# Kernel optimization log

Measured on AMD Instinct MI355X. Metric: run time of the kernel, lower is better.

## Reference

```python
import jax, jax.numpy as jnp
import numpy as np

N_HEAD = 4
HEAD_DIM = 32
D_MODEL = 128
NEG_BIG = -1.0e9  # note: source uses (mask-1)*(-1e9), reproduced faithfully
LN_EPS = 1e-05


def _layer_norm(x, gain, bias):
    mean = jnp.mean(x, axis=-1, keepdims=True)
    var = jnp.mean(jnp.square(x - mean), axis=-1, keepdims=True)
    return gain * (x - mean) / jnp.sqrt(var + LN_EPS) + bias


def setup_inputs() -> dict:
    key = jax.random.key(0)
    ks = jax.random.split(key, 6)
    L, S, D = 8, 2048, D_MODEL
    x = jax.random.normal(ks[0], (L, S, D), dtype=jnp.float32)
    mask = jnp.ones((L, S), dtype=jnp.int32)
    qkv_w = jax.random.normal(ks[1], (D, 3 * D), dtype=jnp.float32) * (1.0 / np.sqrt(D))
    out_w = jax.random.normal(ks[2], (D, D), dtype=jnp.float32) * (1.0 / np.sqrt(D))
    w1 = jax.random.normal(ks[3], (D, 384), dtype=jnp.float32) * (1.0 / np.sqrt(D))
    b1 = jnp.zeros((384,), dtype=jnp.float32)
    w2 = jax.random.normal(ks[4], (384, D), dtype=jnp.float32) * (1.0 / np.sqrt(384))
    b2 = jnp.zeros((D,), dtype=jnp.float32)
    g1 = jnp.ones((D,), dtype=jnp.float32)
    be1 = jnp.zeros((D,), dtype=jnp.float32)
    g2 = jnp.ones((D,), dtype=jnp.float32)
    be2 = jnp.zeros((D,), dtype=jnp.float32)
    return {"x": x, "mask": mask, "qkv_w": qkv_w, "out_w": out_w,
            "w1": w1, "b1": b1, "w2": w2, "b2": b2,
            "g1": g1, "be1": be1, "g2": g2, "be2": be2}


def reference(x, mask, qkv_w, out_w, w1, b1, w2, b2, g1, be1, g2, be2):
    # x: [L, S, D] -- the python list axis of the original module is L (each element batch=1)
    L, S, D = x.shape
    H, hd = N_HEAD, HEAD_DIM
    m = mask.astype(jnp.float32)  # [L, S]

    # QKV projection (single shared weight, split into q/k/v)
    qkv = jnp.einsum('lsd,de->lse', x, qkv_w)  # [L, S, 3D]
    q, k, v = jnp.split(qkv, 3, axis=-1)
    q = q.reshape(L, S, H, hd).transpose(0, 2, 1, 3)  # [L, H, S, hd]
    k = k.reshape(L, S, H, hd).transpose(0, 2, 1, 3)
    v = v.reshape(L, S, H, hd).transpose(0, 2, 1, 3)

    scale = 1.0 / np.sqrt(D // H)
    scores = jnp.einsum('lhqd,lhkd->lhqk', q, k) * scale  # [L, H, S, S]

    # outer-product padding mask, faithful to source: amask*scores + (amask-1)*(-1e9)
    amask = (m[:, None, :, None] * m[:, None, None, :])  # [L, 1, S, S]
    masked = amask * scores + (amask - 1.0) * NEG_BIG
    attn = jax.nn.softmax(masked, axis=-1)

    ctx = jnp.einsum('lhqk,lhkd->lhqd', attn, v)  # [L, H, S, hd]
    ctx = ctx.transpose(0, 2, 1, 3).reshape(L, S, D)
    attn_out = jnp.einsum('lsd,de->lse', ctx, out_w)  # output projection

    # residual + LN1 (dropout rate 0.0 -> identity)
    h = _layer_norm(attn_out + x, g1, be1)

    # FFN: Dense(384, relu) -> Dense(128, relu)
    ff = jax.nn.relu(jnp.einsum('lsd,df->lsf', h, w1) + b1)
    ff = jax.nn.relu(jnp.einsum('lsf,fd->lsd', ff, w2) + b2)

    # residual + LN2
    out = _layer_norm(ff + h, g2, be2)
    return out
```

## Files before the change

kernel.cpp:

```cpp
#include <hip/hip_runtime.h>
#include <hip/hip_bf16.h>

typedef __attribute__((ext_vector_type(8))) short bf16x8;
typedef __attribute__((ext_vector_type(4))) float f32x4;
typedef unsigned short u16;
typedef unsigned int u32;

__device__ __forceinline__ u32 bfr(float x) {
  u32 u = __float_as_uint(x);
  return (u + 0x7fffu + ((u >> 16) & 1u)) >> 16;
}
__device__ __forceinline__ u32 pk2(float lo, float hi) {
  return bfr(lo) | (bfr(hi) << 16);
}
__device__ __forceinline__ u32 cvtpk(float lo, float hi) {
  u32 r;
  asm("v_cvt_pk_bf16_f32 %0, %1, %2" : "=v"(r) : "v"(lo), "v"(hi));
  return r;
}

__device__ __forceinline__ f32x4 mfma16(bf16x8 a, bf16x8 b, f32x4 c) {
  return __builtin_amdgcn_mfma_f32_16x16x32_bf16(a, b, c, 0, 0, 0);
}

__global__ __launch_bounds__(256) void prep_weights(
    const float* __restrict__ qkv_w, const float* __restrict__ out_w,
    const float* __restrict__ w1, const float* __restrict__ w2,
    u16* __restrict__ qkvT, u16* __restrict__ outT,
    u16* __restrict__ w1T, u16* __restrict__ w2T) {
  int idx = blockIdx.x * 256 + threadIdx.x;
  if (idx < 49152) {
    int n = idx >> 7, k = idx & 127;
    qkvT[idx] = (u16)bfr(qkv_w[k * 384 + n]);
  } else if (idx < 49152 + 16384) {
    int i = idx - 49152;
    int n = i >> 7, k = i & 127;
    outT[i] = (u16)bfr(out_w[k * 128 + n]);
  } else if (idx < 49152 + 16384 + 49152) {
    int i = idx - 49152 - 16384;
    int n = i >> 7, k = i & 127;
    w1T[i] = (u16)bfr(w1[k * 384 + n]);
  } else if (idx < 163840) {
    int i = idx - 49152 - 16384 - 49152;
    int n = i / 384, k = i - n * 384;
    w2T[i] = (u16)bfr(w2[k * 128 + n]);
  }
}

__global__ __launch_bounds__(256) void prep_x(const float* __restrict__ x,
                                              u16* __restrict__ xb) {
  int idx = blockIdx.x * 256 + threadIdx.x;
  const float4* p = (const float4*)(x + (size_t)idx * 8);
  float4 a = p[0], b = p[1];
  uint4 w = {pk2(a.x, a.y), pk2(a.z, a.w), pk2(b.x, b.y), pk2(b.z, b.w)};
  *(uint4*)(xb + (size_t)idx * 8) = w;
}

template <int K, int N, int EPI>
__global__ __launch_bounds__(256) void gemm_bf16(
    const u16* __restrict__ A, const u16* __restrict__ WT,
    const float* __restrict__ bias, float* __restrict__ C,
    u16* __restrict__ O0, u16* __restrict__ O1, u16* __restrict__ O2) {
  __shared__ u16 lds_a[64 * 136];
  __shared__ u16 lds_b[64 * 136];
  const int m0 = blockIdx.x * 64, n0 = blockIdx.y * 64;
  const int tid = threadIdx.x, lane = tid & 63, wv = tid >> 6;
  const int wm = wv >> 1, wn = wv & 1, c = lane & 15, g = lane >> 4;

  f32x4 acc[2][2] = {};
  for (int kt = 0; kt < K / 128; ++kt) {
    if (kt) __syncthreads();
    for (int i = tid; i < 1024; i += 256) {
      int row = i >> 4, cc = (i & 15) * 8;
      *(uint4*)(&lds_a[row * 136 + cc]) =
          *(const uint4*)(A + (size_t)(m0 + row) * K + kt * 128 + cc);
      *(uint4*)(&lds_b[row * 136 + cc]) =
          *(const uint4*)(WT + (size_t)(n0 + row) * K + kt * 128 + cc);
    }
    __syncthreads();
#pragma unroll
    for (int ks = 0; ks < 4; ++ks) {
      bf16x8 a0 = *(bf16x8*)(&lds_a[(wm * 32 + c) * 136 + ks * 32 + 8 * g]);
      bf16x8 a1 = *(bf16x8*)(&lds_a[(wm * 32 + 16 + c) * 136 + ks * 32 + 8 * g]);
      bf16x8 b0 = *(bf16x8*)(&lds_b[(wn * 32 + c) * 136 + ks * 32 + 8 * g]);
      bf16x8 b1 = *(bf16x8*)(&lds_b[(wn * 32 + 16 + c) * 136 + ks * 32 + 8 * g]);
      acc[0][0] = mfma16(a0, b0, acc[0][0]);
      acc[0][1] = mfma16(a0, b1, acc[0][1]);
      acc[1][0] = mfma16(a1, b0, acc[1][0]);
      acc[1][1] = mfma16(a1, b1, acc[1][1]);
    }
  }
#pragma unroll
  for (int mi = 0; mi < 2; ++mi)
#pragma unroll
    for (int ni = 0; ni < 2; ++ni) {
      const int n = n0 + wn * 32 + ni * 16 + c;
      const int mb = m0 + wm * 32 + mi * 16 + 4 * g;
      if constexpr (EPI == 0) {
#pragma unroll
        for (int r = 0; r < 4; ++r)
          C[(size_t)(mb + r) * N + n] = acc[mi][ni][r];
      } else if constexpr (EPI == 1) {
        float bv = bias[n];
#pragma unroll
        for (int r = 0; r < 4; ++r)
          C[(size_t)(mb + r) * N + n] = fmaxf(acc[mi][ni][r] + bv, 0.f);
      } else if constexpr (EPI == 2) {
        float bv = bias[n];
#pragma unroll
        for (int r = 0; r < 4; ++r)
          O0[(size_t)(mb + r) * N + n] =
              (u16)bfr(fmaxf(acc[mi][ni][r] + bv, 0.f));
      } else {
        const int reg = n >> 7, hh = (n >> 5) & 3, d = n & 31;
        const int l = mb >> 11, s = mb & 2047;
        const size_t lh = (size_t)l * 4 + hh;
        if (reg == 0) {
#pragma unroll
          for (int r = 0; r < 4; ++r)
            O0[(lh * 2048 + s + r) * 32 + d] =
                (u16)bfr(acc[mi][ni][r] * 0.17677669529663687f);
        } else if (reg == 1) {
#pragma unroll
          for (int r = 0; r < 4; ++r)
            O1[(lh * 2048 + s + r) * 32 + d] = (u16)bfr(acc[mi][ni][r]);
        } else {
          uint2 w = {pk2(acc[mi][ni][0], acc[mi][ni][1]),
                     pk2(acc[mi][ni][2], acc[mi][ni][3])};
          *(uint2*)(O2 + (lh * 32 + d) * 2048 + s) = w;
        }
      }
    }
}

__global__ __launch_bounds__(256) void attn2(
    const u16* __restrict__ Qs, const u16* __restrict__ Kb,
    const u16* __restrict__ Vt, const int* __restrict__ mask,
    u16* __restrict__ ctx) {
  __shared__ u16 lds_k[2][64 * 40];
  __shared__ u16 lds_vt[2][32 * 72];
  __shared__ u16 lds_p[4][16 * 72];
  __shared__ float lds_mk[2][64];

  const int bid = blockIdx.x;
  const int qt = bid & 31, lh = bid >> 5;
  const int tid = threadIdx.x, lane = tid & 63, wv = tid >> 6;
  const int c = lane & 15, g = lane >> 4;
  const int tok0 = (lh >> 2) * 2048;
  const int h = lh & 3;

  const int qrow = qt * 64 + wv * 16 + c;
  const bf16x8 qf = *(const bf16x8*)(Qs + ((size_t)lh * 2048 + qrow) * 32 + 8 * g);
  const float mq = (float)mask[tok0 + qrow];

  const int kr_ = tid & 63, kc_ = tid >> 6;
  const int vr_ = tid >> 3, vc_ = tid & 7;
  const u16* kbase = Kb + ((size_t)lh * 2048) * 32 + kr_ * 32 + kc_ * 8;
  const u16* vbase = Vt + ((size_t)lh * 32 + vr_) * 2048 + vc_ * 8;

  uint4 krg, vrg;
  float mkv;
  auto issue = [&](int kt0) {
    krg = *(const uint4*)(kbase + (size_t)kt0 * 32);
    vrg = *(const uint4*)(vbase + kt0);
    mkv = (tid < 64) ? (float)mask[tok0 + kt0 + tid] : 0.f;
  };
  auto commit = [&](int buf) {
    *(uint4*)(&lds_k[buf][kr_ * 40 + kc_ * 8]) = krg;
    *(uint4*)(&lds_vt[buf][vr_ * 72 + vc_ * 8]) = vrg;
    if (tid < 64) lds_mk[buf][tid] = mkv;
  };

  issue(0);
  commit(0);
  __syncthreads();

  f32x4 acc0 = {0.f, 0.f, 0.f, 0.f}, acc1 = {0.f, 0.f, 0.f, 0.f};
  float m_run = -1e30f, lsum = 0.f;
  const f32x4 zf = {0.f, 0.f, 0.f, 0.f};

  for (int t = 0; t < 32; ++t) {
    const int cur = t & 1;
    if (t < 31) issue((t + 1) * 64);

    f32x4 s[4];
#pragma unroll
    for (int j = 0; j < 4; ++j) {
      bf16x8 a = *(bf16x8*)(&lds_k[cur][(16 * j + c) * 40 + 8 * g]);
      s[j] = mfma16(a, qf, zf);
    }
    float sv[16];
#pragma unroll
    for (int j = 0; j < 4; ++j) {
      float4 mk4 = *(float4*)(&lds_mk[cur][16 * j + 4 * g]);
      const float* mkp = (const float*)&mk4;
#pragma unroll
      for (int r = 0; r < 4; ++r) {
        float am = mq * mkp[r];
        sv[4 * j + r] = am * s[j][r] + (am - 1.0f) * (-1e9f);
      }
    }
    float tmax = sv[0];
#pragma unroll
    for (int i = 1; i < 16; ++i) tmax = fmaxf(tmax, sv[i]);
    tmax = fmaxf(tmax, __shfl_xor(tmax, 16));
    tmax = fmaxf(tmax, __shfl_xor(tmax, 32));
    if (!__all(tmax <= m_run + 8.0f)) {
      float mnew = fmaxf(m_run, tmax);
      float corr = __expf(m_run - mnew);
      m_run = mnew;
      lsum *= corr;
      acc0 *= corr;
      acc1 *= corr;
    }
    float p[16], psum = 0.f;
#pragma unroll
    for (int i = 0; i < 16; ++i) {
      p[i] = __expf(sv[i] - m_run);
      psum += p[i];
    }
    lsum += psum;
#pragma unroll
    for (int j = 0; j < 4; ++j) {
      uint2 w = {cvtpk(p[4 * j], p[4 * j + 1]), cvtpk(p[4 * j + 2], p[4 * j + 3])};
      *(uint2*)(&lds_p[wv][c * 72 + 16 * j + 4 * g]) = w;
    }
    bf16x8 pb0 = *(bf16x8*)(&lds_p[wv][c * 72 + 8 * g]);
    bf16x8 pb1 = *(bf16x8*)(&lds_p[wv][c * 72 + 32 + 8 * g]);
    bf16x8 v00 = *(bf16x8*)(&lds_vt[cur][c * 72 + 8 * g]);
    bf16x8 v01 = *(bf16x8*)(&lds_vt[cur][c * 72 + 32 + 8 * g]);
    bf16x8 v10 = *(bf16x8*)(&lds_vt[cur][(16 + c) * 72 + 8 * g]);
    bf16x8 v11 = *(bf16x8*)(&lds_vt[cur][(16 + c) * 72 + 32 + 8 * g]);
    acc0 = mfma16(v00, pb0, acc0);
    acc0 = mfma16(v01, pb1, acc0);
    acc1 = mfma16(v10, pb0, acc1);
    acc1 = mfma16(v11, pb1, acc1);

    if (t < 31) commit(cur ^ 1);
    __syncthreads();
  }
  float lt = lsum;
  lt += __shfl_xor(lt, 16);
  lt += __shfl_xor(lt, 32);
  float inv = 1.0f / lt;
  u16* op = ctx + (size_t)(tok0 + qrow) * 128 + h * 32;
  uint2 o0 = {cvtpk(acc0[0] * inv, acc0[1] * inv),
              cvtpk(acc0[2] * inv, acc0[3] * inv)};
  uint2 o1 = {cvtpk(acc1[0] * inv, acc1[1] * inv),
              cvtpk(acc1[2] * inv, acc1[3] * inv)};
  *(uint2*)(op + 4 * g) = o0;
  *(uint2*)(op + 16 + 4 * g) = o1;
}

template <bool WB>
__global__ __launch_bounds__(256) void ln_res(
    const float* __restrict__ a, const float* __restrict__ b,
    const float* __restrict__ gain, const float* __restrict__ bias,
    float* __restrict__ out, u16* __restrict__ outb) {
  int token = blockIdx.x * 4 + (threadIdx.x >> 6);
  int lane = threadIdx.x & 63;
  const float2 av = *(const float2*)(a + (size_t)token * 128 + lane * 2);
  const float2 bv = *(const float2*)(b + (size_t)token * 128 + lane * 2);
  float x0 = av.x + bv.x, x1 = av.y + bv.y;
  float s = x0 + x1, q = x0 * x0 + x1 * x1;
#pragma unroll
  for (int off = 32; off >= 1; off >>= 1) {
    s += __shfl_xor(s, off);
    q += __shfl_xor(q, off);
  }
  float mean = s * (1.0f / 128.0f);
  float var = q * (1.0f / 128.0f) - mean * mean;
  float inv = rsqrtf(var + 1e-5f);
  float2 gv = *(const float2*)(gain + lane * 2);
  float2 bev = *(const float2*)(bias + lane * 2);
  float2 o = {gv.x * (x0 - mean) * inv + bev.x,
              gv.y * (x1 - mean) * inv + bev.y};
  *(float2*)(out + (size_t)token * 128 + lane * 2) = o;
  if constexpr (WB)
    *(u32*)(outb + (size_t)token * 128 + lane * 2) = pk2(o.x, o.y);
}

extern "C" void kernel_launch(void* const* d_in, const int* in_sizes, int n_in,
                              void* d_out, int out_size, void* d_ws,
                              size_t ws_size, hipStream_t stream) {
  (void)in_sizes; (void)n_in; (void)out_size; (void)ws_size;
  const float* x = (const float*)d_in[0];
  const int* mask = (const int*)d_in[1];
  const float* qkv_w = (const float*)d_in[2];
  const float* out_w = (const float*)d_in[3];
  const float* w1 = (const float*)d_in[4];
  const float* b1 = (const float*)d_in[5];
  const float* w2 = (const float*)d_in[6];
  const float* b2 = (const float*)d_in[7];
  const float* g1 = (const float*)d_in[8];
  const float* be1 = (const float*)d_in[9];
  const float* g2 = (const float*)d_in[10];
  const float* be2 = (const float*)d_in[11];
  float* out = (float*)d_out;

  char* ws = (char*)d_ws;
  const size_t MB = 1 << 20;
  u16* Qs = (u16*)(ws);
  u16* Kb = (u16*)(ws + 4 * MB);
  u16* Vt = (u16*)(ws + 8 * MB);
  u16* ff_bf = (u16*)(ws);
  u16* ctx_bf = (u16*)(ws + 12 * MB);
  float* attn_out = (float*)(ws + 16 * MB);
  float* ff2 = attn_out;
  float* h = (float*)(ws + 24 * MB);
  u16* h_bf = (u16*)(ws + 32 * MB);
  u16* x_bf = (u16*)(ws + 36 * MB);
  u16* qkvT = (u16*)(ws + 40 * MB);
  u16* outT = qkvT + 384 * 128;
  u16* w1T = outT + 128 * 128;
  u16* w2T = w1T + 384 * 128;

  prep_weights<<<640, 256, 0, stream>>>(qkv_w, out_w, w1, w2, qkvT, outT, w1T, w2T);
  prep_x<<<1024, 256, 0, stream>>>(x, x_bf);
  gemm_bf16<128, 384, 3><<<dim3(256, 6), 256, 0, stream>>>(
      x_bf, qkvT, nullptr, nullptr, Qs, Kb, Vt);
  attn2<<<1024, 256, 0, stream>>>(Qs, Kb, Vt, mask, ctx_bf);
  gemm_bf16<128, 128, 0><<<dim3(256, 2), 256, 0, stream>>>(
      ctx_bf, outT, nullptr, attn_out, nullptr, nullptr, nullptr);
  ln_res<true><<<4096, 256, 0, stream>>>(attn_out, x, g1, be1, h, h_bf);
  gemm_bf16<128, 384, 2><<<dim3(256, 6), 256, 0, stream>>>(
      h_bf, w1T, b1, nullptr, ff_bf, nullptr, nullptr);
  gemm_bf16<384, 128, 1><<<dim3(256, 2), 256, 0, stream>>>(
      ff_bf, w2T, b2, ff2, nullptr, nullptr, nullptr);
  ln_res<false><<<4096, 256, 0, stream>>>(ff2, h, g2, be2, out, nullptr);
}
```

Measured before the change: 114.3 us.

## Fuse residual-add and LayerNorm into full-row output and FFN2 GEMM epilogues

```diff
diff --git a/kernel.cpp b/kernel.cpp
--- a/kernel.cpp
+++ b/kernel.cpp
@@ -59,7 +59,7 @@
 template <int K, int N, int EPI>
 __global__ __launch_bounds__(256) void gemm_bf16(
     const u16* __restrict__ A, const u16* __restrict__ WT,
-    const float* __restrict__ bias, float* __restrict__ C,
+    const float* __restrict__ bias,
     u16* __restrict__ O0, u16* __restrict__ O1, u16* __restrict__ O2) {
   __shared__ u16 lds_a[64 * 136];
   __shared__ u16 lds_b[64 * 136];
@@ -96,16 +96,7 @@
     for (int ni = 0; ni < 2; ++ni) {
       const int n = n0 + wn * 32 + ni * 16 + c;
       const int mb = m0 + wm * 32 + mi * 16 + 4 * g;
-      if constexpr (EPI == 0) {
-#pragma unroll
-        for (int r = 0; r < 4; ++r)
-          C[(size_t)(mb + r) * N + n] = acc[mi][ni][r];
-      } else if constexpr (EPI == 1) {
-        float bv = bias[n];
-#pragma unroll
-        for (int r = 0; r < 4; ++r)
-          C[(size_t)(mb + r) * N + n] = fmaxf(acc[mi][ni][r] + bv, 0.f);
-      } else if constexpr (EPI == 2) {
+      if constexpr (EPI == 2) {
         float bv = bias[n];
 #pragma unroll
         for (int r = 0; r < 4; ++r)
@@ -131,6 +122,86 @@
         }
       }
     }
+}
+
+template <int K, bool RELU>
+__global__ __launch_bounds__(256) void gemm_ln(
+    const u16* __restrict__ A, const u16* __restrict__ WT,
+    const float* __restrict__ bias, const float* __restrict__ resid,
+    const float* __restrict__ gain, const float* __restrict__ lnb,
+    float* __restrict__ outf, u16* __restrict__ outb) {
+  __shared__ u16 lds_a[64 * 136];
+  __shared__ u16 lds_b[128 * 136];
+  const int m0 = blockIdx.x * 64;
+  const int tid = threadIdx.x, lane = tid & 63, wv = tid >> 6;
+  const int c = lane & 15, g = lane >> 4;
+
+  f32x4 acc[8] = {};
+  for (int kt = 0; kt < K / 128; ++kt) {
+    if (kt) __syncthreads();
+    for (int i = tid; i < 1024; i += 256) {
+      int row = i >> 4, cc = (i & 15) * 8;
+      *(uint4*)(&lds_a[row * 136 + cc]) =
+          *(const uint4*)(A + (size_t)(m0 + row) * K + kt * 128 + cc);
+    }
+    for (int i = tid; i < 2048; i += 256) {
+      int row = i >> 4, cc = (i & 15) * 8;
+      *(uint4*)(&lds_b[row * 136 + cc]) =
+          *(const uint4*)(WT + (size_t)row * K + kt * 128 + cc);
+    }
+    __syncthreads();
+#pragma unroll
+    for (int ks = 0; ks < 4; ++ks) {
+      bf16x8 a = *(bf16x8*)(&lds_a[(wv * 16 + c) * 136 + ks * 32 + 8 * g]);
+#pragma unroll
+      for (int ni = 0; ni < 8; ++ni) {
+        bf16x8 b = *(bf16x8*)(&lds_b[(ni * 16 + c) * 136 + ks * 32 + 8 * g]);
+        acc[ni] = mfma16(a, b, acc[ni]);
+      }
+    }
+  }
+  const int rbase = m0 + wv * 16 + 4 * g;
+  float gv[8], lb[8], bv[8];
+#pragma unroll
+  for (int ni = 0; ni < 8; ++ni) {
+    gv[ni] = gain[ni * 16 + c];
+    lb[ni] = lnb[ni * 16 + c];
+    if constexpr (RELU) bv[ni] = bias[ni * 16 + c];
+  }
+  float t[8][4];
+  float sum[4] = {0.f, 0.f, 0.f, 0.f}, sq[4] = {0.f, 0.f, 0.f, 0.f};
+#pragma unroll
+  for (int ni = 0; ni < 8; ++ni) {
+#pragma unroll
+    for (int r = 0; r < 4; ++r) {
+      float v = acc[ni][r];
+      if constexpr (RELU) v = fmaxf(v + bv[ni], 0.f);
+      v += resid[(size_t)(rbase + r) * 128 + ni * 16 + c];
+      t[ni][r] = v;
+      sum[r] += v;
+      sq[r] += v * v;
+    }
+  }
+#pragma unroll
+  for (int off = 1; off < 16; off <<= 1) {
+#pragma unroll
+    for (int r = 0; r < 4; ++r) {
+      sum[r] += __shfl_xor(sum[r], off);
+      sq[r] += __shfl_xor(sq[r], off);
+    }
+  }
+#pragma unroll
+  for (int r = 0; r < 4; ++r) {
+    float mean = sum[r] * (1.0f / 128.0f);
+    float var = sq[r] * (1.0f / 128.0f) - mean * mean;
+    float inv = rsqrtf(var + 1e-5f);
+#pragma unroll
+    for (int ni = 0; ni < 8; ++ni) {
+      float o = gv[ni] * (t[ni][r] - mean) * inv + lb[ni];
+      outf[(size_t)(rbase + r) * 128 + ni * 16 + c] = o;
+      if (outb) outb[(size_t)(rbase + r) * 128 + ni * 16 + c] = (u16)bfr(o);
+    }
+  }
 }
 
 __global__ __launch_bounds__(256) void attn2(
@@ -250,34 +321,6 @@
               cvtpk(acc1[2] * inv, acc1[3] * inv)};
   *(uint2*)(op + 4 * g) = o0;
   *(uint2*)(op + 16 + 4 * g) = o1;
-}
-
-template <bool WB>
-__global__ __launch_bounds__(256) void ln_res(
-    const float* __restrict__ a, const float* __restrict__ b,
-    const float* __restrict__ gain, const float* __restrict__ bias,
-    float* __restrict__ out, u16* __restrict__ outb) {
-  int token = blockIdx.x * 4 + (threadIdx.x >> 6);
-  int lane = threadIdx.x & 63;
-  const float2 av = *(const float2*)(a + (size_t)token * 128 + lane * 2);
-  const float2 bv = *(const float2*)(b + (size_t)token * 128 + lane * 2);
-  float x0 = av.x + bv.x, x1 = av.y + bv.y;
-  float s = x0 + x1, q = x0 * x0 + x1 * x1;
-#pragma unroll
-  for (int off = 32; off >= 1; off >>= 1) {
-    s += __shfl_xor(s, off);
-    q += __shfl_xor(q, off);
-  }
-  float mean = s * (1.0f / 128.0f);
-  float var = q * (1.0f / 128.0f) - mean * mean;
-  float inv = rsqrtf(var + 1e-5f);
-  float2 gv = *(const float2*)(gain + lane * 2);
-  float2 bev = *(const float2*)(bias + lane * 2);
-  float2 o = {gv.x * (x0 - mean) * inv + bev.x,
-              gv.y * (x1 - mean) * inv + bev.y};
-  *(float2*)(out + (size_t)token * 128 + lane * 2) = o;
-  if constexpr (WB)
-    *(u32*)(outb + (size_t)token * 128 + lane * 2) = pk2(o.x, o.y);
 }
 
 extern "C" void kernel_launch(void* const* d_in, const int* in_sizes, int n_in,
@@ -305,12 +348,10 @@
   u16* Vt = (u16*)(ws + 8 * MB);
   u16* ff_bf = (u16*)(ws);
   u16* ctx_bf = (u16*)(ws + 12 * MB);
-  float* attn_out = (float*)(ws + 16 * MB);
-  float* ff2 = attn_out;
-  float* h = (float*)(ws + 24 * MB);
-  u16* h_bf = (u16*)(ws + 32 * MB);
-  u16* x_bf = (u16*)(ws + 36 * MB);
-  u16* qkvT = (u16*)(ws + 40 * MB);
+  float* h = (float*)(ws + 16 * MB);
+  u16* h_bf = (u16*)(ws + 24 * MB);
+  u16* x_bf = (u16*)(ws + 28 * MB);
+  u16* qkvT = (u16*)(ws + 32 * MB);
   u16* outT = qkvT + 384 * 128;
   u16* w1T = outT + 128 * 128;
   u16* w2T = w1T + 384 * 128;
@@ -318,14 +359,12 @@
   prep_weights<<<640, 256, 0, stream>>>(qkv_w, out_w, w1, w2, qkvT, outT, w1T, w2T);
   prep_x<<<1024, 256, 0, stream>>>(x, x_bf);
   gemm_bf16<128, 384, 3><<<dim3(256, 6), 256, 0, stream>>>(
-      x_bf, qkvT, nullptr, nullptr, Qs, Kb, Vt);
+      x_bf, qkvT, nullptr, Qs, Kb, Vt);
   attn2<<<1024, 256, 0, stream>>>(Qs, Kb, Vt, mask, ctx_bf);
-  gemm_bf16<128, 128, 0><<<dim3(256, 2), 256, 0, stream>>>(
-      ctx_bf, outT, nullptr, attn_out, nullptr, nullptr, nullptr);
-  ln_res<true><<<4096, 256, 0, stream>>>(attn_out, x, g1, be1, h, h_bf);
+  gemm_ln<128, false><<<256, 256, 0, stream>>>(
+      ctx_bf, outT, nullptr, x, g1, be1, h, h_bf);
   gemm_bf16<128, 384, 2><<<dim3(256, 6), 256, 0, stream>>>(
-      h_bf, w1T, b1, nullptr, ff_bf, nullptr, nullptr);
-  gemm_bf16<384, 128, 1><<<dim3(256, 2), 256, 0, stream>>>(
-      ff_bf, w2T, b2, ff2, nullptr, nullptr, nullptr);
-  ln_res<false><<<4096, 256, 0, stream>>>(ff2, h, g2, be2, out, nullptr);
-}
+      h_bf, w1T, b1, ff_bf, nullptr, nullptr);
+  gemm_ln<384, true><<<256, 256, 0, stream>>>(
+      ff_bf, w2T, b2, h, g2, be2, out, nullptr);
+}
```

Result: faster. 110.9 us (-3.0%).
